# Kernel tuning notes

Measured on AMD Instinct MI355X. Metric: run time of the kernel, lower is better.

## Reference

```python
import jax, jax.numpy as jnp
import numpy as np

N_WIN = 7    # n_win hardcoded in AR_Attention
TOPK = 4     # topk routing windows
HEADS = 8    # num_heads


def setup_inputs() -> dict:
    key = jax.random.key(0)
    ks = jax.random.split(key, 6)
    B, H, W, C = 4, 56, 56, 256
    s = 0.02
    x = jax.random.normal(ks[0], (B, H, W, C), jnp.float32)
    Wqkv = jax.random.normal(ks[1], (C, 3 * C), jnp.float32) * s  # Linear(dim, 3*dim) (qk_dim=dim)
    bqkv = jnp.zeros((3 * C,), jnp.float32)
    Wo = jax.random.normal(ks[2], (C, C), jnp.float32) * s        # output projection Linear(dim, dim)
    bo = jnp.zeros((C,), jnp.float32)
    lepe_w = jax.random.normal(ks[3], (5, 5, 1, C), jnp.float32) * s  # 5x5 depthwise conv (side_dwconv=5)
    lepe_b = jnp.zeros((C,), jnp.float32)
    return {"x": x, "Wqkv": Wqkv, "bqkv": bqkv, "Wo": Wo, "bo": bo,
            "lepe_w": lepe_w, "lepe_b": lepe_b}


def reference(x, Wqkv, bqkv, Wo, bo, lepe_w, lepe_b):
    B, H, W, C = x.shape
    nw = N_WIN
    h, w = H // nw, W // nw           # region size (8x8)
    p2 = nw * nw                      # number of regions (49)
    hd = C // HEADS                   # head dim
    scale = float(C) ** -0.5          # qk_scale = qk_dim ** -0.5 (qk_dim = dim)

    # region partition: [B,H,W,C] -> [B,p2,h,w,C]
    xr = x.reshape(B, nw, h, nw, w, C).transpose(0, 1, 3, 2, 4, 5).reshape(B, p2, h, w, C)

    qkv = xr @ Wqkv + bqkv            # [B,p2,h,w,3C]
    q, kv = qkv[..., :C], qkv[..., C:]

    q_pix = q.reshape(B, p2, h * w, C)
    kv_pix = kv.reshape(B, p2, h * w, 2 * C)   # kv_downsample_mode='identity'

    # region-level queries/keys via per-window mean pooling
    q_win = q.mean((2, 3))                     # [B,p2,C]
    k_win = kv[..., :C].mean((2, 3))           # [B,p2,C]

    # LEPE: 5x5 depthwise conv on v over the full image grid
    v_img = kv[..., C:].reshape(B, nw, nw, h, w, C).transpose(0, 1, 3, 2, 4, 5).reshape(B, H, W, C)
    lepe = jax.lax.conv_general_dilated(
        v_img, lepe_w, (1, 1), 'SAME',
        dimension_numbers=('NHWC', 'HWIO', 'NHWC'),
        feature_group_count=C) + lepe_b

    # top-k window routing (param_routing=False, hard routing, mul_weight='none')
    r_logit = jnp.einsum('bpc,bqc->bpq', q_win * scale, k_win)  # [B,p2,p2]
    _, r_idx = jax.lax.top_k(r_logit, TOPK)                     # [B,p2,TOPK]

    # gather selected kv windows: [B,p2,TOPK,h*w,2C]
    kv_sel = jax.vmap(lambda kvp, i: kvp[i])(kv_pix, r_idx)

    k_sel = kv_sel[..., :C].reshape(B, p2, TOPK * h * w, HEADS, hd)
    v_sel = kv_sel[..., C:].reshape(B, p2, TOPK * h * w, HEADS, hd)
    qh = q_pix.reshape(B, p2, h * w, HEADS, hd)

    attn = jnp.einsum('bpqnd,bpknd->bpnqk', qh * scale, k_sel)  # [B,p2,heads,hw,TOPK*hw]
    attn = jax.nn.softmax(attn, axis=-1)
    out = jnp.einsum('bpnqk,bpknd->bpqnd', attn, v_sel).reshape(B, p2, h, w, C)

    # windows back to image grid
    out = out.reshape(B, nw, nw, h, w, C).transpose(0, 1, 3, 2, 4, 5).reshape(B, H, W, C)
    out = out + lepe
    return out @ Wo + bo
```

## Files before the change

### kernel.cpp

```cpp
#include <hip/hip_runtime.h>
#include <hip/hip_bf16.h>

#define NPIX 12544

typedef short bf16x8 __attribute__((ext_vector_type(8)));
typedef float f32x4  __attribute__((ext_vector_type(4)));

__device__ __forceinline__ float bf2f(unsigned short u) {
    unsigned int x = ((unsigned int)u) << 16;
    float f; __builtin_memcpy(&f, &x, sizeof(f)); return f;
}
__device__ __forceinline__ unsigned short f2bf(float f) {
    __hip_bfloat16 h = __float2bfloat16(f);
    unsigned short u; __builtin_memcpy(&u, &h, 2); return u;
}
__device__ __forceinline__ void load_lds16(const unsigned short* g, unsigned short* l) {
    __builtin_amdgcn_global_load_lds(
        (const __attribute__((address_space(1))) unsigned int*)g,
        (__attribute__((address_space(3))) unsigned int*)l,
        16, 0, 0);
}

__global__ __launch_bounds__(256) void k_prep(
    const float* __restrict__ X, unsigned short* __restrict__ Xb,
    float* __restrict__ xmean,
    const float* __restrict__ Wqkv, const float* __restrict__ Wo,
    unsigned short* __restrict__ Wtq, unsigned short* __restrict__ Wto)
{
    __shared__ __align__(16) unsigned char sm[64 * 65 * 4];
    const int t = threadIdx.x;
    const int blk = blockIdx.x;
    if (blk < 196) {
        float* part = (float*)sm;
        const int b = blk / 49, p = blk % 49;
        const int wi = p / 7, wj = p % 7;
        const int ps = t >> 6, cg = t & 63;
        float4 s = {0.f, 0.f, 0.f, 0.f};
        #pragma unroll
        for (int i = 0; i < 16; i++) {
            int pp = ps * 16 + i;
            int y = wi * 8 + (pp >> 3), x = wj * 8 + (pp & 7);
            int idx = (((b * 56) + y) * 56 + x) * 256 + cg * 4;
            float4 v = *reinterpret_cast<const float4*>(X + idx);
            s.x += v.x; s.y += v.y; s.z += v.z; s.w += v.w;
            ushort4 o = { f2bf(v.x), f2bf(v.y), f2bf(v.z), f2bf(v.w) };
            *reinterpret_cast<ushort4*>(Xb + idx) = o;
        }
        *reinterpret_cast<float4*>(part + t * 4) = *reinterpret_cast<float4*>(&s);
        __syncthreads();
        if (t < 64) {
            float4 a = *reinterpret_cast<float4*>(part + t * 4);
            float4 b2 = *reinterpret_cast<float4*>(part + (64 + t) * 4);
            float4 c = *reinterpret_cast<float4*>(part + (128 + t) * 4);
            float4 d = *reinterpret_cast<float4*>(part + (192 + t) * 4);
            float4 m = { (a.x + b2.x + c.x + d.x) * (1.f / 64.f),
                         (a.y + b2.y + c.y + d.y) * (1.f / 64.f),
                         (a.z + b2.z + c.z + d.z) * (1.f / 64.f),
                         (a.w + b2.w + c.w + d.w) * (1.f / 64.f) };
            *reinterpret_cast<float4*>(xmean + blk * 256 + t * 4) = m;
        }
    } else {
        float* tile = (float*)sm;
        int tb = blk - 196;
        const float* Wsrc; unsigned short* Wdst; int N, kt, nt;
        if (tb < 48) { Wsrc = Wqkv; Wdst = Wtq; N = 768; kt = tb / 12; nt = tb % 12; }
        else { tb -= 48; Wsrc = Wo; Wdst = Wto; N = 256; kt = tb / 4; nt = tb % 4; }
        const int k0 = kt * 64, n0 = nt * 64;
        const int r0 = t >> 6, c = t & 63;
        #pragma unroll
        for (int i = 0; i < 16; i++) {
            int r = i * 4 + r0;
            tile[r * 65 + c] = Wsrc[(size_t)(k0 + r) * N + n0 + c];
        }
        __syncthreads();
        #pragma unroll
        for (int i = 0; i < 16; i++) {
            int n = i * 4 + r0;
            Wdst[(size_t)(n0 + n) * 256 + k0 + c] = f2bf(tile[c * 65 + n]);
        }
    }
}

__global__ __launch_bounds__(256) void k_qkv_gemm(
    const unsigned short* __restrict__ A,
    const unsigned short* __restrict__ Bt,
    const float* __restrict__ bias,
    unsigned short* __restrict__ O)
{
    __shared__ unsigned short As[128 * 32];
    __shared__ unsigned short Bs[128 * 32];
    const int t = threadIdx.x;
    const int m0 = blockIdx.x * 128, n0 = blockIdx.y * 128;
    const int wave = t >> 6, lane = t & 63, quad = lane >> 4, lo = lane & 15;
    const int wm = wave & 1, wn = wave >> 1;
    const int sr = wave * 16 + (lane >> 2);
    const int sc = lane & 3;
    f32x4 acc[4][4];
    #pragma unroll
    for (int i = 0; i < 4; i++)
        #pragma unroll
        for (int j = 0; j < 4; j++) acc[i][j] = (f32x4){0.f, 0.f, 0.f, 0.f};

    for (int kt = 0; kt < 256; kt += 32) {
        __syncthreads();
        #pragma unroll
        for (int j = 0; j < 2; j++) {
            int row = j * 64 + sr;
            int e = sc ^ ((row >> 1) & 3);
            load_lds16(A  + (size_t)(m0 + row) * 256 + kt + e * 8, &As[row * 32 + sc * 8]);
            load_lds16(Bt + (size_t)(n0 + row) * 256 + kt + e * 8, &Bs[row * 32 + sc * 8]);
        }
        __syncthreads();
        bf16x8 af[4], bfr[4];
        #pragma unroll
        for (int mt = 0; mt < 4; mt++) {
            int row = wm * 64 + mt * 16 + lo;
            int c = quad ^ ((row >> 1) & 3);
            af[mt] = *reinterpret_cast<const bf16x8*>(&As[row * 32 + c * 8]);
        }
        #pragma unroll
        for (int nt = 0; nt < 4; nt++) {
            int col = wn * 64 + nt * 16 + lo;
            int c = quad ^ ((col >> 1) & 3);
            bfr[nt] = *reinterpret_cast<const bf16x8*>(&Bs[col * 32 + c * 8]);
        }
        #pragma unroll
        for (int mt = 0; mt < 4; mt++)
            #pragma unroll
            for (int nt = 0; nt < 4; nt++)
                acc[mt][nt] = __builtin_amdgcn_mfma_f32_16x16x32_bf16(
                    af[mt], bfr[nt], acc[mt][nt], 0, 0, 0);
    }
    float bv[4];
    #pragma unroll
    for (int nt = 0; nt < 4; nt++) bv[nt] = bias[n0 + wn * 64 + nt * 16 + lo];
    #pragma unroll
    for (int mt = 0; mt < 4; mt++)
        #pragma unroll
        for (int nt = 0; nt < 4; nt++) {
            int n = n0 + wn * 64 + nt * 16 + lo;
            #pragma unroll
            for (int r = 0; r < 4; r++) {
                int m = m0 + wm * 64 + mt * 16 + quad * 4 + r;
                O[m * 768 + n] = f2bf(acc[mt][nt][r] + bv[nt]);
            }
        }
}

__global__ __launch_bounds__(256) void k_winproj(
    const float* __restrict__ xmean,
    const float* __restrict__ W,
    const float* __restrict__ bias,
    float* __restrict__ qwin, float* __restrict__ kwin)
{
    __shared__ float xs[256];
    const int bp = blockIdx.x;
    const int half = blockIdx.y;
    const int c = threadIdx.x;
    xs[c] = xmean[bp * 256 + c];
    __syncthreads();
    const int col = half * 256 + c;
    float a = 0.f;
    for (int k = 0; k < 256; k++) a += xs[k] * W[k * 768 + col];
    float* outp = half ? kwin : qwin;
    outp[bp * 256 + c] = a + bias[col];
}

__global__ __launch_bounds__(256) void k_route(
    const float* __restrict__ qwin, const float* __restrict__ kwin,
    int* __restrict__ ridx)
{
    __shared__ float part[49][4];
    __shared__ float lg[49];
    const int bp = blockIdx.x;
    const int b = bp / 49, p = bp % 49;
    const int t = threadIdx.x;
    if (t < 196) {
        int d = t >> 2, pr = t & 3;
        const float* qp = &qwin[(b * 49 + p) * 256];
        const float* kp = &kwin[(b * 49 + d) * 256];
        float a = 0.f;
        for (int ch = pr * 64; ch < pr * 64 + 64; ch++) a += qp[ch] * kp[ch];
        part[d][pr] = a;
    }
    __syncthreads();
    if (t < 49) lg[t] = (part[t][0] + part[t][1] + part[t][2] + part[t][3]);
    __syncthreads();
    if (t == 0) {
        unsigned long long used = 0ull;
        for (int sel = 0; sel < 4; sel++) {
            float best = -1e30f; int bi = 0;
            for (int qq = 0; qq < 49; qq++)
                if (!((used >> qq) & 1ull) && lg[qq] > best) { best = lg[qq]; bi = qq; }
            used |= (1ull << bi);
            ridx[bp * 4 + sel] = bi;
        }
    }
}

__global__ __launch_bounds__(256) void k_lepe(
    const unsigned short* __restrict__ QKV,
    const float* __restrict__ lw, const float* __restrict__ lb,
    unsigned short* __restrict__ Olepe)
{
    __shared__ float lws[25 * 256];
    const int t = threadIdx.x;
    #pragma unroll
    for (int i = 0; i < 25; i++) lws[i * 256 + t] = lw[i * 256 + t];

    const int pl = t & 7;
    const int cg = t >> 3;
    const int c0 = cg * 8;
    const int gid = blockIdx.x * 8 + pl;
    const int b = gid / 3136, rem = gid % 3136;
    const int y = rem / 56, x = rem % 56;
    __syncthreads();

    float acc[8];
    {
        float4 b0 = *reinterpret_cast<const float4*>(lb + c0);
        float4 b1 = *reinterpret_cast<const float4*>(lb + c0 + 4);
        acc[0] = b0.x; acc[1] = b0.y; acc[2] = b0.z; acc[3] = b0.w;
        acc[4] = b1.x; acc[5] = b1.y; acc[6] = b1.z; acc[7] = b1.w;
    }
    #pragma unroll
    for (int ky = 0; ky < 5; ky++) {
        int yy = y + ky - 2;
        if (yy < 0 || yy >= 56) continue;
        #pragma unroll
        for (int kx = 0; kx < 5; kx++) {
            int xx = x + kx - 2;
            if (xx < 0 || xx >= 56) continue;
            bf16x8 v = *reinterpret_cast<const bf16x8*>(
                QKV + (((b * 56) + yy) * 56 + xx) * 768 + 512 + c0);
            const float* wrow = &lws[(ky * 5 + kx) * 256 + c0];
            float4 w0 = *reinterpret_cast<const float4*>(wrow);
            float4 w1 = *reinterpret_cast<const float4*>(wrow + 4);
            acc[0] += bf2f((unsigned short)v[0]) * w0.x;
            acc[1] += bf2f((unsigned short)v[1]) * w0.y;
            acc[2] += bf2f((unsigned short)v[2]) * w0.z;
            acc[3] += bf2f((unsigned short)v[3]) * w0.w;
            acc[4] += bf2f((unsigned short)v[4]) * w1.x;
            acc[5] += bf2f((unsigned short)v[5]) * w1.y;
            acc[6] += bf2f((unsigned short)v[6]) * w1.z;
            acc[7] += bf2f((unsigned short)v[7]) * w1.w;
        }
    }
    bf16x8 o;
    #pragma unroll
    for (int j = 0; j < 8; j++) o[j] = (short)f2bf(acc[j]);
    *reinterpret_cast<bf16x8*>(Olepe + (size_t)gid * 256 + c0) = o;
}

__global__ __launch_bounds__(256) void k_attn(
    const unsigned short* __restrict__ QKV,
    const int* __restrict__ ridx,
    const unsigned short* __restrict__ Olepe,
    unsigned short* __restrict__ Osum)
{
    __shared__ __align__(16) unsigned char smem[50688];
    unsigned short* Vt = (unsigned short*)smem;
    unsigned short* Qs = (unsigned short*)(smem + 16896);
    unsigned short* Ks = (unsigned short*)(smem + 22016);
    unsigned short* Ps = (unsigned short*)(smem + 16896);

    const int p = blockIdx.x, head = blockIdx.y, b = blockIdx.z;
    const int t = threadIdx.x;
    const int wi = p / 7, wj = p % 7;
    const int wave = t >> 6, lane = t & 63, quad = lane >> 4, lo = lane & 15;
    const int pix4 = t >> 2, c4 = t & 3;

    {
        int y = wi * 8 + (pix4 >> 3), x = wj * 8 + (pix4 & 7);
        const unsigned short* qp = QKV + (((b * 56) + y) * 56 + x) * 768 + head * 32 + c4 * 8;
        bf16x8 v = *reinterpret_cast<const bf16x8*>(qp);
        int sw = c4 ^ ((pix4 >> 3) & 3);
        *reinterpret_cast<bf16x8*>(&Qs[pix4 * 40 + sw * 8]) = v;
    }
    #pragma unroll
    for (int pass = 0; pass < 4; pass++) {
        int sel = ridx[(b * 49 + p) * 4 + pass];
        int si = sel / 7, sj = sel % 7;
        int y = si * 8 + (pix4 >> 3), x = sj * 8 + (pix4 & 7);
        const unsigned short* base = QKV + (((b * 56) + y) * 56 + x) * 768 + 256 + head * 32;
        bf16x8 kv = *reinterpret_cast<const bf16x8*>(base + c4 * 8);
        bf16x8 vv = *reinterpret_cast<const bf16x8*>(base + 256 + c4 * 8);
        int krow = pass * 64 + pix4;
        int sw = c4 ^ ((krow >> 3) & 3);
        *reinterpret_cast<bf16x8*>(&Ks[krow * 40 + sw * 8]) = kv;
        #pragma unroll
        for (int j = 0; j < 8; j++)
            Vt[(c4 * 8 + j) * 264 + krow] = (unsigned short)vv[j];
    }
    __syncthreads();

    f32x4 sc[16];
    {
        int row = wave * 16 + lo;
        bf16x8 af = *reinterpret_cast<const bf16x8*>(
            &Qs[row * 40 + ((quad ^ ((row >> 3) & 3)) * 8)]);
        f32x4 z = (f32x4){0.f, 0.f, 0.f, 0.f};
        #pragma unroll
        for (int nt = 0; nt < 16; nt++) {
            int key = nt * 16 + lo;
            bf16x8 bfr = *reinterpret_cast<const bf16x8*>(
                &Ks[key * 40 + ((quad ^ ((key >> 3) & 3)) * 8)]);
            sc[nt] = __builtin_amdgcn_mfma_f32_16x16x32_bf16(af, bfr, z, 0, 0, 0);
        }
    }
    float M[4] = {-1e30f, -1e30f, -1e30f, -1e30f};
    #pragma unroll
    for (int nt = 0; nt < 16; nt++)
        #pragma unroll
        for (int r = 0; r < 4; r++) M[r] = fmaxf(M[r], sc[nt][r] * 0.0625f);
    #pragma unroll
    for (int d = 1; d < 16; d <<= 1)
        #pragma unroll
        for (int r = 0; r < 4; r++) M[r] = fmaxf(M[r], __shfl_xor(M[r], d));
    float l[4] = {0.f, 0.f, 0.f, 0.f};
    #pragma unroll
    for (int nt = 0; nt < 16; nt++)
        #pragma unroll
        for (int r = 0; r < 4; r++) {
            float e = __expf(sc[nt][r] * 0.0625f - M[r]);
            sc[nt][r] = e;
            l[r] += e;
        }
    #pragma unroll
    for (int d = 1; d < 16; d <<= 1)
        #pragma unroll
        for (int r = 0; r < 4; r++) l[r] += __shfl_xor(l[r], d);

    __syncthreads();

    unsigned short* myPs = Ps + wave * 16 * 264;
    #pragma unroll
    for (int nt = 0; nt < 16; nt++)
        #pragma unroll
        for (int r = 0; r < 4; r++)
            myPs[(quad * 4 + r) * 264 + nt * 16 + lo] = f2bf(sc[nt][r]);

    f32x4 o0 = (f32x4){0.f, 0.f, 0.f, 0.f}, o1 = o0;
    #pragma unroll
    for (int kt = 0; kt < 8; kt++) {
        bf16x8 pa = *reinterpret_cast<const bf16x8*>(
            &myPs[lo * 264 + kt * 32 + quad * 8]);
        bf16x8 vb0 = *reinterpret_cast<const bf16x8*>(
            &Vt[lo * 264 + kt * 32 + quad * 8]);
        bf16x8 vb1 = *reinterpret_cast<const bf16x8*>(
            &Vt[(16 + lo) * 264 + kt * 32 + quad * 8]);
        o0 = __builtin_amdgcn_mfma_f32_16x16x32_bf16(pa, vb0, o0, 0, 0, 0);
        o1 = __builtin_amdgcn_mfma_f32_16x16x32_bf16(pa, vb1, o1, 0, 0, 0);
    }
    #pragma unroll
    for (int r = 0; r < 4; r++) {
        int q = wave * 16 + quad * 4 + r;
        int y = wi * 8 + (q >> 3), x = wj * 8 + (q & 7);
        size_t base = (size_t)(((b * 56) + y) * 56 + x) * 256 + head * 32;
        const unsigned short* lp = Olepe + base;
        unsigned short* op = Osum + base;
        float inv = 1.0f / l[r];
        op[lo]      = f2bf(o0[r] * inv + bf2f(lp[lo]));
        op[16 + lo] = f2bf(o1[r] * inv + bf2f(lp[16 + lo]));
    }
}

__global__ __launch_bounds__(256) void k_proj(
    const unsigned short* __restrict__ A,
    const unsigned short* __restrict__ Bt,
    const float* __restrict__ bias,
    float* __restrict__ O)
{
    __shared__ unsigned short As[128 * 32];
    __shared__ unsigned short Bs[64 * 32];
    const int t = threadIdx.x;
    const int m0 = blockIdx.x * 128, n0 = blockIdx.y * 64;
    const int wave = t >> 6, lane = t & 63, quad = lane >> 4, lo = lane & 15;
    const int sr = wave * 16 + (lane >> 2);
    const int sc = lane & 3;
    f32x4 acc[2][4];
    #pragma unroll
    for (int i = 0; i < 2; i++)
        #pragma unroll
        for (int j = 0; j < 4; j++) acc[i][j] = (f32x4){0.f, 0.f, 0.f, 0.f};

    for (int kt = 0; kt < 256; kt += 32) {
        __syncthreads();
        #pragma unroll
        for (int j = 0; j < 2; j++) {
            int row = j * 64 + sr;
            int e = sc ^ ((row >> 1) & 3);
            load_lds16(A + (size_t)(m0 + row) * 256 + kt + e * 8, &As[row * 32 + sc * 8]);
        }
        {
            int e = sc ^ ((sr >> 1) & 3);
            load_lds16(Bt + (size_t)(n0 + sr) * 256 + kt + e * 8, &Bs[sr * 32 + sc * 8]);
        }
        __syncthreads();
        bf16x8 af[2], bfr[4];
        #pragma unroll
        for (int mt = 0; mt < 2; mt++) {
            int row = wave * 32 + mt * 16 + lo;
            int c = quad ^ ((row >> 1) & 3);
            af[mt] = *reinterpret_cast<const bf16x8*>(&As[row * 32 + c * 8]);
        }
        #pragma unroll
        for (int nt = 0; nt < 4; nt++) {
            int col = nt * 16 + lo;
            int c = quad ^ ((col >> 1) & 3);
            bfr[nt] = *reinterpret_cast<const bf16x8*>(&Bs[col * 32 + c * 8]);
        }
        #pragma unroll
        for (int mt = 0; mt < 2; mt++)
            #pragma unroll
            for (int nt = 0; nt < 4; nt++)
                acc[mt][nt] = __builtin_amdgcn_mfma_f32_16x16x32_bf16(
                    af[mt], bfr[nt], acc[mt][nt], 0, 0, 0);
    }
    float bv[4];
    #pragma unroll
    for (int nt = 0; nt < 4; nt++) bv[nt] = bias[n0 + nt * 16 + lo];
    #pragma unroll
    for (int mt = 0; mt < 2; mt++)
        #pragma unroll
        for (int nt = 0; nt < 4; nt++) {
            int n = n0 + nt * 16 + lo;
            #pragma unroll
            for (int r = 0; r < 4; r++) {
                int m = m0 + wave * 32 + mt * 16 + quad * 4 + r;
                O[m * 256 + n] = acc[mt][nt][r] + bv[nt];
            }
        }
}

extern "C" void kernel_launch(void* const* d_in, const int* in_sizes, int n_in,
                              void* d_out, int out_size, void* d_ws, size_t ws_size,
                              hipStream_t stream)
{
    const float* x    = (const float*)d_in[0];
    const float* Wqkv = (const float*)d_in[1];
    const float* bqkv = (const float*)d_in[2];
    const float* Wo   = (const float*)d_in[3];
    const float* bo   = (const float*)d_in[4];
    const float* lw   = (const float*)d_in[5];
    const float* lb   = (const float*)d_in[6];
    float* out = (float*)d_out;

    char* ws = (char*)d_ws;
    size_t off = 0;
    unsigned short* qkv   = (unsigned short*)(ws + off); off += (size_t)NPIX * 768 * 2;
    unsigned short* xb    = (unsigned short*)(ws + off); off += (size_t)NPIX * 256 * 2;
    unsigned short* Wtq   = (unsigned short*)(ws + off); off += 768 * 256 * 2;
    unsigned short* Wto   = (unsigned short*)(ws + off); off += 256 * 256 * 2;
    unsigned short* Osum  = (unsigned short*)(ws + off); off += (size_t)NPIX * 256 * 2;
    unsigned short* Olepe = (unsigned short*)(ws + off); off += (size_t)NPIX * 256 * 2;
    float* xmean = (float*)(ws + off); off += 196 * 256 * 4;
    float* qwin  = (float*)(ws + off); off += 196 * 256 * 4;
    float* kwin  = (float*)(ws + off); off += 196 * 256 * 4;
    int*   ridx  = (int*)(ws + off);   off += 196 * 4 * 4;

    k_prep    <<<dim3(260),      256, 0, stream>>>(x, xb, xmean, Wqkv, Wo, Wtq, Wto);
    k_qkv_gemm<<<dim3(98, 6),    256, 0, stream>>>(xb, Wtq, bqkv, qkv);
    k_winproj <<<dim3(196, 2),   256, 0, stream>>>(xmean, Wqkv, bqkv, qwin, kwin);
    k_route   <<<dim3(196),      256, 0, stream>>>(qwin, kwin, ridx);
    k_lepe    <<<dim3(1568),     256, 0, stream>>>(qkv, lw, lb, Olepe);
    k_attn    <<<dim3(49, 8, 4), 256, 0, stream>>>(qkv, ridx, Olepe, Osum);
    k_proj    <<<dim3(98, 4),    256, 0, stream>>>(Osum, Wto, bo, out);
}
```

Measured before the change: 168.2 us.

## Merge independent kernels into combined launches and split prep blocks by channel half

Merges the QKV GEMM with the window-mean projection into one launch, and routing with the LEPE depthwise conv into another, using block-index ranges to dispatch. This cuts the pipeline from seven launches to five, removing launch gaps and letting the small, low-occupancy kernels run alongside the larger ones. The prep kernel also splits each window into two channel halves, doubling its block count for better parallelism. The cost is a larger shared-memory footprint for the merged kernels, since each reserves the maximum of its branches, plus divergent per-block code paths.

```diff
diff --git a/kernel.cpp b/kernel.cpp
--- a/kernel.cpp
+++ b/kernel.cpp
@@ -30,17 +30,19 @@
     __shared__ __align__(16) unsigned char sm[64 * 65 * 4];
     const int t = threadIdx.x;
     const int blk = blockIdx.x;
-    if (blk < 196) {
+    if (blk < 392) {
         float* part = (float*)sm;
-        const int b = blk / 49, p = blk % 49;
+        const int w = blk >> 1, hc = blk & 1;
+        const int b = w / 49, p = w % 49;
         const int wi = p / 7, wj = p % 7;
-        const int ps = t >> 6, cg = t & 63;
+        const int ch0 = hc * 128;
+        const int ps = t >> 5, cg = t & 31;
         float4 s = {0.f, 0.f, 0.f, 0.f};
         #pragma unroll
-        for (int i = 0; i < 16; i++) {
-            int pp = ps * 16 + i;
+        for (int i = 0; i < 8; i++) {
+            int pp = ps * 8 + i;
             int y = wi * 8 + (pp >> 3), x = wj * 8 + (pp & 7);
-            int idx = (((b * 56) + y) * 56 + x) * 256 + cg * 4;
+            int idx = (((b * 56) + y) * 56 + x) * 256 + ch0 + cg * 4;
             float4 v = *reinterpret_cast<const float4*>(X + idx);
             s.x += v.x; s.y += v.y; s.z += v.z; s.w += v.w;
             ushort4 o = { f2bf(v.x), f2bf(v.y), f2bf(v.z), f2bf(v.w) };
@@ -48,20 +50,20 @@
         }
         *reinterpret_cast<float4*>(part + t * 4) = *reinterpret_cast<float4*>(&s);
         __syncthreads();
-        if (t < 64) {
-            float4 a = *reinterpret_cast<float4*>(part + t * 4);
-            float4 b2 = *reinterpret_cast<float4*>(part + (64 + t) * 4);
-            float4 c = *reinterpret_cast<float4*>(part + (128 + t) * 4);
-            float4 d = *reinterpret_cast<float4*>(part + (192 + t) * 4);
-            float4 m = { (a.x + b2.x + c.x + d.x) * (1.f / 64.f),
-                         (a.y + b2.y + c.y + d.y) * (1.f / 64.f),
-                         (a.z + b2.z + c.z + d.z) * (1.f / 64.f),
-                         (a.w + b2.w + c.w + d.w) * (1.f / 64.f) };
-            *reinterpret_cast<float4*>(xmean + blk * 256 + t * 4) = m;
+        if (t < 32) {
+            float4 m = {0.f, 0.f, 0.f, 0.f};
+            #pragma unroll
+            for (int ps2 = 0; ps2 < 8; ps2++) {
+                float4 v = *reinterpret_cast<float4*>(part + (ps2 * 32 + t) * 4);
+                m.x += v.x; m.y += v.y; m.z += v.z; m.w += v.w;
+            }
+            m.x *= (1.f / 64.f); m.y *= (1.f / 64.f);
+            m.z *= (1.f / 64.f); m.w *= (1.f / 64.f);
+            *reinterpret_cast<float4*>(xmean + w * 256 + ch0 + t * 4) = m;
         }
     } else {
         float* tile = (float*)sm;
-        int tb = blk - 196;
+        int tb = blk - 392;
         const float* Wsrc; unsigned short* Wdst; int N, kt, nt;
         if (tb < 48) { Wsrc = Wqkv; Wdst = Wtq; N = 768; kt = tb / 12; nt = tb % 12; }
         else { tb -= 48; Wsrc = Wo; Wdst = Wto; N = 256; kt = tb / 4; nt = tb % 4; }
@@ -81,175 +83,175 @@
     }
 }
 
-__global__ __launch_bounds__(256) void k_qkv_gemm(
+__global__ __launch_bounds__(256) void k_main1(
     const unsigned short* __restrict__ A,
     const unsigned short* __restrict__ Bt,
     const float* __restrict__ bias,
-    unsigned short* __restrict__ O)
-{
-    __shared__ unsigned short As[128 * 32];
-    __shared__ unsigned short Bs[128 * 32];
+    unsigned short* __restrict__ O,
+    const float* __restrict__ xmean,
+    const float* __restrict__ Wqkv,
+    float* __restrict__ qwin, float* __restrict__ kwin)
+{
+    __shared__ __align__(16) unsigned char sm1[16384];
     const int t = threadIdx.x;
-    const int m0 = blockIdx.x * 128, n0 = blockIdx.y * 128;
-    const int wave = t >> 6, lane = t & 63, quad = lane >> 4, lo = lane & 15;
-    const int wm = wave & 1, wn = wave >> 1;
-    const int sr = wave * 16 + (lane >> 2);
-    const int sc = lane & 3;
-    f32x4 acc[4][4];
-    #pragma unroll
-    for (int i = 0; i < 4; i++)
-        #pragma unroll
-        for (int j = 0; j < 4; j++) acc[i][j] = (f32x4){0.f, 0.f, 0.f, 0.f};
-
-    for (int kt = 0; kt < 256; kt += 32) {
-        __syncthreads();
-        #pragma unroll
-        for (int j = 0; j < 2; j++) {
-            int row = j * 64 + sr;
-            int e = sc ^ ((row >> 1) & 3);
-            load_lds16(A  + (size_t)(m0 + row) * 256 + kt + e * 8, &As[row * 32 + sc * 8]);
-            load_lds16(Bt + (size_t)(n0 + row) * 256 + kt + e * 8, &Bs[row * 32 + sc * 8]);
-        }
-        __syncthreads();
-        bf16x8 af[4], bfr[4];
-        #pragma unroll
-        for (int mt = 0; mt < 4; mt++) {
-            int row = wm * 64 + mt * 16 + lo;
-            int c = quad ^ ((row >> 1) & 3);
-            af[mt] = *reinterpret_cast<const bf16x8*>(&As[row * 32 + c * 8]);
-        }
-        #pragma unroll
-        for (int nt = 0; nt < 4; nt++) {
-            int col = wn * 64 + nt * 16 + lo;
-            int c = quad ^ ((col >> 1) & 3);
-            bfr[nt] = *reinterpret_cast<const bf16x8*>(&Bs[col * 32 + c * 8]);
-        }
+    const int blk = blockIdx.x;
+    if (blk < 588) {
+        unsigned short* As = (unsigned short*)sm1;
+        unsigned short* Bs = (unsigned short*)(sm1 + 8192);
+        const int m0 = (blk % 98) * 128, n0 = (blk / 98) * 128;
+        const int wave = t >> 6, lane = t & 63, quad = lane >> 4, lo = lane & 15;
+        const int wm = wave & 1, wn = wave >> 1;
+        const int sr = wave * 16 + (lane >> 2);
+        const int sc = lane & 3;
+        f32x4 acc[4][4];
+        #pragma unroll
+        for (int i = 0; i < 4; i++)
+            #pragma unroll
+            for (int j = 0; j < 4; j++) acc[i][j] = (f32x4){0.f, 0.f, 0.f, 0.f};
+
+        for (int kt = 0; kt < 256; kt += 32) {
+            __syncthreads();
+            #pragma unroll
+            for (int j = 0; j < 2; j++) {
+                int row = j * 64 + sr;
+                int e = sc ^ ((row >> 1) & 3);
+                load_lds16(A  + (size_t)(m0 + row) * 256 + kt + e * 8, &As[row * 32 + sc * 8]);
+                load_lds16(Bt + (size_t)(n0 + row) * 256 + kt + e * 8, &Bs[row * 32 + sc * 8]);
+            }
+            __syncthreads();
+            bf16x8 af[4], bfr[4];
+            #pragma unroll
+            for (int mt = 0; mt < 4; mt++) {
+                int row = wm * 64 + mt * 16 + lo;
+                int c = quad ^ ((row >> 1) & 3);
+                af[mt] = *reinterpret_cast<const bf16x8*>(&As[row * 32 + c * 8]);
+            }
+            #pragma unroll
+            for (int nt = 0; nt < 4; nt++) {
+                int col = wn * 64 + nt * 16 + lo;
+                int c = quad ^ ((col >> 1) & 3);
+                bfr[nt] = *reinterpret_cast<const bf16x8*>(&Bs[col * 32 + c * 8]);
+            }
+            #pragma unroll
+            for (int mt = 0; mt < 4; mt++)
+                #pragma unroll
+                for (int nt = 0; nt < 4; nt++)
+                    acc[mt][nt] = __builtin_amdgcn_mfma_f32_16x16x32_bf16(
+                        af[mt], bfr[nt], acc[mt][nt], 0, 0, 0);
+        }
+        float bv[4];
+        #pragma unroll
+        for (int nt = 0; nt < 4; nt++) bv[nt] = bias[n0 + wn * 64 + nt * 16 + lo];
         #pragma unroll
         for (int mt = 0; mt < 4; mt++)
             #pragma unroll
-            for (int nt = 0; nt < 4; nt++)
-                acc[mt][nt] = __builtin_amdgcn_mfma_f32_16x16x32_bf16(
-                    af[mt], bfr[nt], acc[mt][nt], 0, 0, 0);
-    }
-    float bv[4];
-    #pragma unroll
-    for (int nt = 0; nt < 4; nt++) bv[nt] = bias[n0 + wn * 64 + nt * 16 + lo];
-    #pragma unroll
-    for (int mt = 0; mt < 4; mt++)
-        #pragma unroll
-        for (int nt = 0; nt < 4; nt++) {
-            int n = n0 + wn * 64 + nt * 16 + lo;
-            #pragma unroll
-            for (int r = 0; r < 4; r++) {
-                int m = m0 + wm * 64 + mt * 16 + quad * 4 + r;
-                O[m * 768 + n] = f2bf(acc[mt][nt][r] + bv[nt]);
-            }
-        }
-}
-
-__global__ __launch_bounds__(256) void k_winproj(
-    const float* __restrict__ xmean,
-    const float* __restrict__ W,
-    const float* __restrict__ bias,
-    float* __restrict__ qwin, float* __restrict__ kwin)
-{
-    __shared__ float xs[256];
-    const int bp = blockIdx.x;
-    const int half = blockIdx.y;
-    const int c = threadIdx.x;
-    xs[c] = xmean[bp * 256 + c];
-    __syncthreads();
-    const int col = half * 256 + c;
-    float a = 0.f;
-    for (int k = 0; k < 256; k++) a += xs[k] * W[k * 768 + col];
-    float* outp = half ? kwin : qwin;
-    outp[bp * 256 + c] = a + bias[col];
-}
-
-__global__ __launch_bounds__(256) void k_route(
+            for (int nt = 0; nt < 4; nt++) {
+                int n = n0 + wn * 64 + nt * 16 + lo;
+                #pragma unroll
+                for (int r = 0; r < 4; r++) {
+                    int m = m0 + wm * 64 + mt * 16 + quad * 4 + r;
+                    O[m * 768 + n] = f2bf(acc[mt][nt][r] + bv[nt]);
+                }
+            }
+    } else {
+        float* xs = (float*)sm1;
+        const int u = blk - 588;
+        const int bp = u % 196;
+        const int half = u / 196;
+        const int c = t;
+        xs[c] = xmean[bp * 256 + c];
+        __syncthreads();
+        const int col = half * 256 + c;
+        float a = 0.f;
+        for (int k = 0; k < 256; k++) a += xs[k] * Wqkv[k * 768 + col];
+        float* outp = half ? kwin : qwin;
+        outp[bp * 256 + c] = a + bias[col];
+    }
+}
+
+__global__ __launch_bounds__(256) void k_main2(
     const float* __restrict__ qwin, const float* __restrict__ kwin,
-    int* __restrict__ ridx)
-{
-    __shared__ float part[49][4];
-    __shared__ float lg[49];
-    const int bp = blockIdx.x;
-    const int b = bp / 49, p = bp % 49;
-    const int t = threadIdx.x;
-    if (t < 196) {
-        int d = t >> 2, pr = t & 3;
-        const float* qp = &qwin[(b * 49 + p) * 256];
-        const float* kp = &kwin[(b * 49 + d) * 256];
-        float a = 0.f;
-        for (int ch = pr * 64; ch < pr * 64 + 64; ch++) a += qp[ch] * kp[ch];
-        part[d][pr] = a;
-    }
-    __syncthreads();
-    if (t < 49) lg[t] = (part[t][0] + part[t][1] + part[t][2] + part[t][3]);
-    __syncthreads();
-    if (t == 0) {
-        unsigned long long used = 0ull;
-        for (int sel = 0; sel < 4; sel++) {
-            float best = -1e30f; int bi = 0;
-            for (int qq = 0; qq < 49; qq++)
-                if (!((used >> qq) & 1ull) && lg[qq] > best) { best = lg[qq]; bi = qq; }
-            used |= (1ull << bi);
-            ridx[bp * 4 + sel] = bi;
-        }
-    }
-}
-
-__global__ __launch_bounds__(256) void k_lepe(
+    int* __restrict__ ridx,
     const unsigned short* __restrict__ QKV,
     const float* __restrict__ lw, const float* __restrict__ lb,
     unsigned short* __restrict__ Olepe)
 {
-    __shared__ float lws[25 * 256];
+    __shared__ __align__(16) unsigned char sm2[25600];
     const int t = threadIdx.x;
-    #pragma unroll
-    for (int i = 0; i < 25; i++) lws[i * 256 + t] = lw[i * 256 + t];
-
-    const int pl = t & 7;
-    const int cg = t >> 3;
-    const int c0 = cg * 8;
-    const int gid = blockIdx.x * 8 + pl;
-    const int b = gid / 3136, rem = gid % 3136;
-    const int y = rem / 56, x = rem % 56;
-    __syncthreads();
-
-    float acc[8];
-    {
-        float4 b0 = *reinterpret_cast<const float4*>(lb + c0);
-        float4 b1 = *reinterpret_cast<const float4*>(lb + c0 + 4);
-        acc[0] = b0.x; acc[1] = b0.y; acc[2] = b0.z; acc[3] = b0.w;
-        acc[4] = b1.x; acc[5] = b1.y; acc[6] = b1.z; acc[7] = b1.w;
-    }
-    #pragma unroll
-    for (int ky = 0; ky < 5; ky++) {
-        int yy = y + ky - 2;
-        if (yy < 0 || yy >= 56) continue;
-        #pragma unroll
-        for (int kx = 0; kx < 5; kx++) {
-            int xx = x + kx - 2;
-            if (xx < 0 || xx >= 56) continue;
-            bf16x8 v = *reinterpret_cast<const bf16x8*>(
-                QKV + (((b * 56) + yy) * 56 + xx) * 768 + 512 + c0);
-            const float* wrow = &lws[(ky * 5 + kx) * 256 + c0];
-            float4 w0 = *reinterpret_cast<const float4*>(wrow);
-            float4 w1 = *reinterpret_cast<const float4*>(wrow + 4);
-            acc[0] += bf2f((unsigned short)v[0]) * w0.x;
-            acc[1] += bf2f((unsigned short)v[1]) * w0.y;
-            acc[2] += bf2f((unsigned short)v[2]) * w0.z;
-            acc[3] += bf2f((unsigned short)v[3]) * w0.w;
-            acc[4] += bf2f((unsigned short)v[4]) * w1.x;
-            acc[5] += bf2f((unsigned short)v[5]) * w1.y;
-            acc[6] += bf2f((unsigned short)v[6]) * w1.z;
-            acc[7] += bf2f((unsigned short)v[7]) * w1.w;
-        }
-    }
-    bf16x8 o;
-    #pragma unroll
-    for (int j = 0; j < 8; j++) o[j] = (short)f2bf(acc[j]);
-    *reinterpret_cast<bf16x8*>(Olepe + (size_t)gid * 256 + c0) = o;
+    const int blk = blockIdx.x;
+    if (blk < 196) {
+        float* part = (float*)sm2;
+        float* lg   = (float*)(sm2 + 49 * 4 * 4);
+        const int b = blk / 49, p = blk % 49;
+        if (t < 196) {
+            int d = t >> 2, pr = t & 3;
+            const float* qp = &qwin[(b * 49 + p) * 256];
+            const float* kp = &kwin[(b * 49 + d) * 256];
+            float a = 0.f;
+            for (int ch = pr * 64; ch < pr * 64 + 64; ch++) a += qp[ch] * kp[ch];
+            part[d * 4 + pr] = a;
+        }
+        __syncthreads();
+        if (t < 49) lg[t] = part[t * 4 + 0] + part[t * 4 + 1] + part[t * 4 + 2] + part[t * 4 + 3];
+        __syncthreads();
+        if (t == 0) {
+            unsigned long long used = 0ull;
+            for (int sel = 0; sel < 4; sel++) {
+                float best = -1e30f; int bi = 0;
+                for (int qq = 0; qq < 49; qq++)
+                    if (!((used >> qq) & 1ull) && lg[qq] > best) { best = lg[qq]; bi = qq; }
+                used |= (1ull << bi);
+                ridx[blk * 4 + sel] = bi;
+            }
+        }
+    } else {
+        float* lws = (float*)sm2;
+        #pragma unroll
+        for (int i = 0; i < 25; i++) lws[i * 256 + t] = lw[i * 256 + t];
+
+        const int pl = t & 7;
+        const int cg = t >> 3;
+        const int c0 = cg * 8;
+        const int gid = (blk - 196) * 8 + pl;
+        const int b = gid / 3136, rem = gid % 3136;
+        const int y = rem / 56, x = rem % 56;
+        __syncthreads();
+
+        float acc[8];
+        {
+            float4 b0 = *reinterpret_cast<const float4*>(lb + c0);
+            float4 b1 = *reinterpret_cast<const float4*>(lb + c0 + 4);
+            acc[0] = b0.x; acc[1] = b0.y; acc[2] = b0.z; acc[3] = b0.w;
+            acc[4] = b1.x; acc[5] = b1.y; acc[6] = b1.z; acc[7] = b1.w;
+        }
+        #pragma unroll
+        for (int ky = 0; ky < 5; ky++) {
+            int yy = y + ky - 2;
+            if (yy < 0 || yy >= 56) continue;
+            #pragma unroll
+            for (int kx = 0; kx < 5; kx++) {
+                int xx = x + kx - 2;
+                if (xx < 0 || xx >= 56) continue;
+                bf16x8 v = *reinterpret_cast<const bf16x8*>(
+                    QKV + (((b * 56) + yy) * 56 + xx) * 768 + 512 + c0);
+                const float* wrow = &lws[(ky * 5 + kx) * 256 + c0];
+                float4 w0 = *reinterpret_cast<const float4*>(wrow);
+                float4 w1 = *reinterpret_cast<const float4*>(wrow + 4);
+                acc[0] += bf2f((unsigned short)v[0]) * w0.x;
+                acc[1] += bf2f((unsigned short)v[1]) * w0.y;
+                acc[2] += bf2f((unsigned short)v[2]) * w0.z;
+                acc[3] += bf2f((unsigned short)v[3]) * w0.w;
+                acc[4] += bf2f((unsigned short)v[4]) * w1.x;
+                acc[5] += bf2f((unsigned short)v[5]) * w1.y;
+                acc[6] += bf2f((unsigned short)v[6]) * w1.z;
+                acc[7] += bf2f((unsigned short)v[7]) * w1.w;
+            }
+        }
+        bf16x8 o;
+        #pragma unroll
+        for (int j = 0; j < 8; j++) o[j] = (short)f2bf(acc[j]);
+        *reinterpret_cast<bf16x8*>(Olepe + (size_t)gid * 256 + c0) = o;
+    }
 }
 
 __global__ __launch_bounds__(256) void k_attn(
@@ -459,11 +461,9 @@
     float* kwin  = (float*)(ws + off); off += 196 * 256 * 4;
     int*   ridx  = (int*)(ws + off);   off += 196 * 4 * 4;
 
-    k_prep    <<<dim3(260),      256, 0, stream>>>(x, xb, xmean, Wqkv, Wo, Wtq, Wto);
-    k_qkv_gemm<<<dim3(98, 6),    256, 0, stream>>>(xb, Wtq, bqkv, qkv);
-    k_winproj <<<dim3(196, 2),   256, 0, stream>>>(xmean, Wqkv, bqkv, qwin, kwin);
-    k_route   <<<dim3(196),      256, 0, stream>>>(qwin, kwin, ridx);
-    k_lepe    <<<dim3(1568),     256, 0, stream>>>(qkv, lw, lb, Olepe);
-    k_attn    <<<dim3(49, 8, 4), 256, 0, stream>>>(qkv, ridx, Olepe, Osum);
-    k_proj    <<<dim3(98, 4),    256, 0, stream>>>(Osum, Wto, bo, out);
-}
+    k_prep <<<dim3(456),      256, 0, stream>>>(x, xb, xmean, Wqkv, Wo, Wtq, Wto);
+    k_main1<<<dim3(980),      256, 0, stream>>>(xb, Wtq, bqkv, qkv, xmean, Wqkv, qwin, kwin);
+    k_main2<<<dim3(1764),     256, 0, stream>>>(qwin, kwin, ridx, qkv, lw, lb, Olepe);
+    k_attn <<<dim3(49, 8, 4), 256, 0, stream>>>(qkv, ridx, Olepe, Osum);
+    k_proj <<<dim3(98, 4),    256, 0, stream>>>(Osum, Wto, bo, out);
+}
```

After: 153.2 us. 1.1x faster.
